# Performance work log

Measured on AMD Instinct MI355X. Metric: run time of the kernel, lower is better.

Reference implementation:

```python
import jax, jax.numpy as jnp
import numpy as np

K = 6  # kernel size for all locally connected layers

def lc2d(x, w, b, stride):
    # x: [B,C,H,W]; w: [O,C,oh,ow,K*K]; b: [O,oh,ow]
    oh, ow = w.shape[2], w.shape[3]
    s = stride
    # unfold: stack the K*K shifted strided views -> [B,C,oh,ow,K*K]
    patches = jnp.stack([x[:, :, i:i + (oh - 1) * s + 1:s, j:j + (ow - 1) * s + 1:s]
                         for i in range(K) for j in range(K)], axis=-1)
    out = jnp.einsum('bchwk,ochwk->bohw', patches, w)
    return out + b[None]

def maxpool2(x):
    # MaxPool2d(2), floor mode: crop odd trailing row/col then 2x2 max
    B, C, H, W = x.shape
    x = x[:, :, : (H // 2) * 2, : (W // 2) * 2]
    return x.reshape(B, C, H // 2, 2, W // 2, 2).max(axis=(3, 5))

def setup_inputs() -> dict:
    key = jax.random.key(0)
    ks = jax.random.split(key, 9)
    f = lambda k, sh: jax.random.normal(k, sh, dtype=jnp.float32) * 0.05
    return {
        'x':  jax.random.normal(ks[0], (16, 3, 218, 178), dtype=jnp.float32),
        'w1': f(ks[1], (8, 3, 213, 173, 36)),  'b1': f(ks[2], (8, 213, 173)),
        'w2': f(ks[3], (16, 8, 51, 41, 36)),   'b2': f(ks[4], (16, 51, 41)),
        'w3': f(ks[5], (32, 16, 16, 12, 36)),  'b3': f(ks[6], (32, 16, 12)),
        'wf': f(ks[7], (10178, 6144)),         'bf': f(ks[8], (10178,)),
    }

def reference(x, w1, b1, w2, b2, w3, b3, wf, bf):
    h = jax.nn.relu(lc2d(x, w1, b1, stride=1))   # [B,8,213,173]
    h = maxpool2(h)                               # [B,8,106,86]
    h = jax.nn.relu(lc2d(h, w2, b2, stride=2))   # [B,16,51,41]
    h = jax.nn.relu(lc2d(h, w3, b3, stride=3))   # [B,32,16,12]
    h = h.reshape(h.shape[0], -1)                 # [B,6144]
    return h @ wf.T + bf                          # [B,10178]
```

## Files before the change

kernel.cpp:

```cpp
#include <hip/hip_runtime.h>

static __device__ __forceinline__ void fma4(float4& a, float s, float4 v) {
  a.x = fmaf(s, v.x, a.x);
  a.y = fmaf(s, v.y, a.y);
  a.z = fmaf(s, v.z, a.z);
  a.w = fmaf(s, v.w, a.w);
}
static __device__ __forceinline__ float4 relu4(float4 a) {
  return make_float4(fmaxf(a.x, 0.f), fmaxf(a.y, 0.f),
                     fmaxf(a.z, 0.f), fmaxf(a.w, 0.f));
}
typedef float floatv4 __attribute__((ext_vector_type(4)));
static __device__ __forceinline__ float4 ntld4(const float* p) {
  floatv4 v = __builtin_nontemporal_load(reinterpret_cast<const floatv4*>(p));
  return make_float4(v.x, v.y, v.z, v.w);
}
typedef float f32x4v __attribute__((ext_vector_type(4)));
typedef short bf16x8 __attribute__((ext_vector_type(8)));
static __device__ __forceinline__ unsigned short f2bf(float f) {
  unsigned u = __float_as_uint(f);
  return (unsigned short)((u + 0x7FFFu + ((u >> 16) & 1u)) >> 16);
}

__global__ void k_transpose(const float* __restrict__ x, float* __restrict__ xt,
                            int chw, int total) {
  int p = blockIdx.x * blockDim.x + threadIdx.x;
  if (p >= total) return;
  float v[16];
#pragma unroll
  for (int b = 0; b < 16; ++b) v[b] = x[(size_t)b * chw + p];
  float4* o4 = reinterpret_cast<float4*>(xt) + (size_t)p * 4;
#pragma unroll
  for (int q = 0; q < 4; ++q)
    o4[q] = make_float4(v[4 * q + 0], v[4 * q + 1], v[4 * q + 2], v[4 * q + 3]);
}

__global__ __launch_bounds__(256, 4) void k_lc1_mfma(
    const float* __restrict__ xt, const float* __restrict__ wgt,
    const float* __restrict__ bias, float* __restrict__ out) {
  constexpr int C = 3, IH = 218, IW = 178, OH = 213, OW = 173;
  constexpr int POS = OH * OW;
  constexpr int KP = 136;
  constexpr int CSTR = IH * IW * 16;
  __shared__ unsigned short wl[16 * 8 * KP];

  const int tid = threadIdx.x;
  const int p0 = blockIdx.x * 16;

  for (int i = tid; i < 3456; i += 256) {
    int pos = i / 216;
    int r = i % 216;
    int o = r / 27;
    int rr = r % 27;
    int c = rr / 9;
    int g4 = rr % 9;
    int gpos = p0 + pos;
    if (gpos >= POS) gpos = POS - 1;
    float4 v = *reinterpret_cast<const float4*>(
        wgt + ((size_t)(o * C + c) * POS + gpos) * 36 + g4 * 4);
    int k0 = (g4 < 8) ? (c * 32 + g4 * 4) : (96 + c * 4);
    unsigned short* d = &wl[(pos * 8 + o) * KP + k0];
    d[0] = f2bf(v.x); d[1] = f2bf(v.y); d[2] = f2bf(v.z); d[3] = f2bf(v.w);
  }
  for (int i = tid; i < 3584; i += 256) {
    int row = i / 28;
    int q = i % 28;
    wl[row * KP + 108 + q] = 0;
  }
  __syncthreads();

  const int l = tid & 63;
  const int wid = tid >> 6;
  const int g = l >> 4;
  const int bb = l & 15;
  const int orow = l & 7;

  int base[8];
  int off3[8];
  bool v3[8];
#pragma unroll
  for (int j = 0; j < 8; ++j) {
    int tap = g * 8 + j;
    base[j] = ((tap / 6) * IW + (tap % 6)) * 16;
    int q = g * 8 + j;
    bool v = (q < 12);
    int cc = v ? (q >> 2) : 0;
    int t3 = v ? (32 + (q & 3)) : 32;
    off3[j] = (cc * IH + 5) * IW * 16 + ((t3 - 30)) * 16;
    v3[j] = v;
  }

  for (int pp = 0; pp < 4; ++pp) {
    int gpos = p0 + wid * 4 + pp;
    bool valid = gpos < POS;
    int cg = valid ? gpos : POS - 1;
    int h = cg / OW, w = cg % OW;
    int posoff = (h * IW + w) * 16 + bb;
    int lpos = wid * 4 + pp;

    f32x4v acc;
#pragma unroll
    for (int j = 0; j < 4; ++j) {
      int o = g * 4 + j;
      acc[j] = (g < 2) ? bias[(size_t)o * POS + cg] : 0.f;
    }

#pragma unroll
    for (int ch = 0; ch < 4; ++ch) {
      bf16x8 a = *reinterpret_cast<const bf16x8*>(
          &wl[(lpos * 8 + orow) * KP + ch * 32 + g * 8]);
      bf16x8 b;
#pragma unroll
      for (int j = 0; j < 8; ++j) {
        float xv;
        if (ch < 3)
          xv = xt[posoff + ch * CSTR + base[j]];
        else
          xv = v3[j] ? xt[posoff + off3[j]] : 0.f;
        b[j] = (short)f2bf(xv);
      }
      acc = __builtin_amdgcn_mfma_f32_16x16x32_bf16(a, b, acc, 0, 0, 0);
    }

    if (valid && g < 2) {
#pragma unroll
      for (int j = 0; j < 4; ++j) {
        int o = g * 4 + j;
        out[((size_t)o * POS + cg) * 16 + bb] = fmaxf(acc[j], 0.f);
      }
    }
  }
}

template <int C, int IH, int IW, int OH, int OW, int S, int O_TOT>
__global__ __launch_bounds__(256) void k_lc_lds_part(
    const float* __restrict__ xt, const float* __restrict__ wgt,
    float* __restrict__ part) {
  constexpr int POS = OH * OW;
  constexpr int NT = (POS + 63) / 64;
  constexpr int OGN = O_TOT / 4;
  __shared__ float4 wl[4 * 64 * 9];
  int tile = blockIdx.x % NT;
  int rem = blockIdx.x / NT;
  int ob0 = (rem % OGN) * 4;
  int c = rem / OGN;
  int p0 = tile * 64;
  int PN = (POS - p0) < 64 ? (POS - p0) : 64;
  int lp = threadIdx.x >> 2, bq = threadIdx.x & 3;
  int fp = p0 + lp;
  bool act = lp < PN;
  int h = act ? fp / OW : 0;
  int w = act ? fp % OW : 0;

  const float4* x4 = reinterpret_cast<const float4*>(xt);
  const float4* w4 = reinterpret_cast<const float4*>(wgt);

  for (int i = threadIdx.x; i < 2304; i += 256) {
    int o_l = i / 576;
    int r = i % 576;
    int pos = r / 9;
    int k4 = r % 9;
    if (pos < PN)
      wl[(o_l * 64 + pos) * 9 + k4] =
          w4[((size_t)((ob0 + o_l) * C + c) * POS + p0 + pos) * 9 + k4];
  }
  __syncthreads();
  if (!act) return;

  float4 acc[4];
#pragma unroll
  for (int o = 0; o < 4; ++o) acc[o] = make_float4(0.f, 0.f, 0.f, 0.f);

  const float4* xc = x4 + ((size_t)(c * IH + h * S) * IW + w * S) * 4 + bq;
#pragma unroll
  for (int k4 = 0; k4 < 9; ++k4) {
    float4 xv[4];
#pragma unroll
    for (int r = 0; r < 4; ++r) {
      int k = k4 * 4 + r;
      xv[r] = xc[((k / 6) * IW + (k % 6)) * 4];
    }
#pragma unroll
    for (int o = 0; o < 4; ++o) {
      float4 wv = wl[(o * 64 + lp) * 9 + k4];
      fma4(acc[o], wv.x, xv[0]);
      fma4(acc[o], wv.y, xv[1]);
      fma4(acc[o], wv.z, xv[2]);
      fma4(acc[o], wv.w, xv[3]);
    }
  }
  float4* pp = reinterpret_cast<float4*>(part) + (size_t)c * (O_TOT * POS * 4);
#pragma unroll
  for (int o = 0; o < 4; ++o)
    pp[((size_t)(ob0 + o) * POS + fp) * 4 + bq] = acc[o];
}

template <int CC, bool A3T>
__global__ void k_combine(const float* __restrict__ part,
                          const float* __restrict__ bias,
                          float* __restrict__ out, int n4total) {
  int p = blockIdx.x * blockDim.x + threadIdx.x;
  if (p >= n4total) return;
  const float4* p4 = reinterpret_cast<const float4*>(part);
  float4 acc = make_float4(0.f, 0.f, 0.f, 0.f);
#pragma unroll
  for (int c = 0; c < CC; ++c) {
    float4 v = p4[(size_t)c * n4total + p];
    acc.x += v.x; acc.y += v.y; acc.z += v.z; acc.w += v.w;
  }
  float bv = bias[p >> 2];
  acc = relu4(make_float4(acc.x + bv, acc.y + bv, acc.z + bv, acc.w + bv));
  if (A3T) {
    int k = p >> 2;
    int bq = p & 3;
    out[(size_t)(bq * 4 + 0) * 6144 + k] = acc.x;
    out[(size_t)(bq * 4 + 1) * 6144 + k] = acc.y;
    out[(size_t)(bq * 4 + 2) * 6144 + k] = acc.z;
    out[(size_t)(bq * 4 + 3) * 6144 + k] = acc.w;
  } else {
    reinterpret_cast<float4*>(out)[p] = acc;
  }
}

__global__ void k_pool(const float* __restrict__ in, float* __restrict__ out,
                       int IH, int IW, int PH, int PW, int total) {
  int t = blockIdx.x * blockDim.x + threadIdx.x;
  if (t >= total) return;
  int bq = t & 3;
  int p = t >> 2;
  int w = p % PW; p /= PW;
  int h = p % PH; p /= PH;
  int o = p;
  const float4* in4 = reinterpret_cast<const float4*>(in);
  size_t r0 = ((size_t)(o * IH + 2 * h) * IW + 2 * w) * 4 + bq;
  float4 a = in4[r0];
  float4 b = in4[r0 + 4];
  float4 c = in4[r0 + (size_t)IW * 4];
  float4 d = in4[r0 + (size_t)IW * 4 + 4];
  float4 m;
  m.x = fmaxf(fmaxf(a.x, b.x), fmaxf(c.x, d.x));
  m.y = fmaxf(fmaxf(a.y, b.y), fmaxf(c.y, d.y));
  m.z = fmaxf(fmaxf(a.z, b.z), fmaxf(c.z, d.z));
  m.w = fmaxf(fmaxf(a.w, b.w), fmaxf(c.w, d.w));
  reinterpret_cast<float4*>(out)[((size_t)(o * PH + h) * PW + w) * 4 + bq] = m;
}

constexpr int FC_N = 10178;
constexpr int FC_K = 6144;
constexpr int FC_KC = 2;
constexpr int FC_KLEN = FC_K / FC_KC;

__global__ __launch_bounds__(256) void k_fc(const float* __restrict__ a3t,
                                            const float* __restrict__ wf,
                                            float* __restrict__ fcp) {
  int wv = threadIdx.x >> 6;
  int l = threadIdx.x & 63;
  int n0 = (blockIdx.x * 4 + wv) * 4;
  int kc = blockIdx.y;
  int kbase = kc * FC_KLEN;

  float acc[64];
#pragma unroll
  for (int j = 0; j < 64; ++j) acc[j] = 0.f;

  int n[4];
#pragma unroll
  for (int m = 0; m < 4; ++m) {
    int nn = n0 + m;
    n[m] = nn < FC_N ? nn : FC_N - 1;
  }

  float4 wr[4];
  {
    int k = kbase + 4 * l;
#pragma unroll
    for (int m = 0; m < 4; ++m) wr[m] = ntld4(wf + (size_t)n[m] * FC_K + k);
  }

  for (int k0 = 0; k0 < FC_KLEN; k0 += 256) {
    int k = kbase + k0 + 4 * l;
    int kp = (k0 + 256 < FC_KLEN) ? (k + 256) : (kbase + 4 * l);
    float4 wrn[4];
#pragma unroll
    for (int m = 0; m < 4; ++m) wrn[m] = ntld4(wf + (size_t)n[m] * FC_K + kp);

#pragma unroll
    for (int bg = 0; bg < 4; ++bg) {
      float4 xv[4];
#pragma unroll
      for (int r = 0; r < 4; ++r)
        xv[r] = *reinterpret_cast<const float4*>(a3t +
                    (size_t)(bg * 4 + r) * FC_K + k);
#pragma unroll
      for (int r = 0; r < 4; ++r) {
        int b = bg * 4 + r;
#pragma unroll
        for (int m = 0; m < 4; ++m) {
          int j = b * 4 + m;
          acc[j] = fmaf(wr[m].x, xv[r].x, acc[j]);
          acc[j] = fmaf(wr[m].y, xv[r].y, acc[j]);
          acc[j] = fmaf(wr[m].z, xv[r].z, acc[j]);
          acc[j] = fmaf(wr[m].w, xv[r].w, acc[j]);
        }
      }
      __builtin_amdgcn_sched_barrier(0);
    }
#pragma unroll
    for (int m = 0; m < 4; ++m) wr[m] = wrn[m];
  }

#pragma unroll
  for (int s = 0; s < 6; ++s) {
    int mask = 1 << s;
    int bit = (l >> s) & 1;
#pragma unroll
    for (int t = 0; t < 32; ++t) {
      if (t < (64 >> (s + 1))) {
        float e = acc[2 * t] + __shfl_xor(acc[2 * t], mask, 64);
        float o = acc[2 * t + 1] + __shfl_xor(acc[2 * t + 1], mask, 64);
        acc[t] = bit ? o : e;
      }
    }
  }

  int b = l >> 2;
  int m = l & 3;
  int nn = n0 + m;
  if (nn < FC_N)
    fcp[((size_t)kc * 16 + b) * FC_N + nn] = acc[0];
}

__global__ void k_fc_comb(const float* __restrict__ fcp,
                          const float* __restrict__ bf,
                          float* __restrict__ out, int total) {
  int t = blockIdx.x * blockDim.x + threadIdx.x;
  if (t >= total) return;
  unsigned n = (unsigned)t % (unsigned)FC_N;
  float s = bf[n];
#pragma unroll
  for (int kc = 0; kc < FC_KC; ++kc) s += fcp[(size_t)kc * 16 * FC_N + t];
  out[t] = s;
}

static inline int cdiv(int a, int b) { return (a + b - 1) / b; }

extern "C" void kernel_launch(void* const* d_in, const int* in_sizes, int n_in,
                              void* d_out, int out_size, void* d_ws,
                              size_t ws_size, hipStream_t stream) {
  const float* x  = (const float*)d_in[0];
  const float* w1 = (const float*)d_in[1];
  const float* b1 = (const float*)d_in[2];
  const float* w2 = (const float*)d_in[3];
  const float* b2 = (const float*)d_in[4];
  const float* w3 = (const float*)d_in[5];
  const float* b3 = (const float*)d_in[6];
  const float* wf = (const float*)d_in[7];
  const float* bf = (const float*)d_in[8];
  float* out = (float*)d_out;

  float* ws = (float*)d_ws;
  float* xt     = ws;
  float* a1     = ws + 1862592;
  float* a1p    = ws + 6579264;
  float* a2     = ws + 7746112;
  float* a3t    = ws + 8281408;
  float* l2part = a1;
  float* l3part = xt;
  float* fcp    = a1p;

  {
    int total = 3 * 218 * 178;
    k_transpose<<<cdiv(total, 256), 256, 0, stream>>>(x, xt, total, total);
  }
  {
    k_lc1_mfma<<<cdiv(213 * 173, 16), 256, 0, stream>>>(xt, w1, b1, a1);
  }
  {
    int total = 4 * 8 * 106 * 86;
    k_pool<<<cdiv(total, 256), 256, 0, stream>>>(a1, a1p, 213, 173, 106, 86,
                                                 total);
  }
  {
    k_lc_lds_part<8, 106, 86, 51, 41, 2, 16>
        <<<33 * 4 * 8, 256, 0, stream>>>(a1p, w2, l2part);
  }
  {
    int n4 = 16 * 2091 * 4;
    k_combine<8, false><<<cdiv(n4, 256), 256, 0, stream>>>(l2part, b2, a2, n4);
  }
  {
    k_lc_lds_part<16, 51, 41, 16, 12, 3, 32>
        <<<3 * 8 * 16, 256, 0, stream>>>(a2, w3, l3part);
  }
  {
    int n4 = 32 * 192 * 4;
    k_combine<16, true><<<cdiv(n4, 256), 256, 0, stream>>>(l3part, b3, a3t, n4);
  }
  {
    dim3 grid(cdiv(FC_N, 16), FC_KC);
    k_fc<<<grid, 256, 0, stream>>>(a3t, wf, fcp);
  }
  {
    int total = 16 * FC_N;
    k_fc_comb<<<cdiv(total, 256), 256, 0, stream>>>(fcp, bf, out, total);
  }
}
```

Baseline: 181.5 us.

## Stage layer-1 input window in LDS as bf16 with row-aligned position tiles

Layer-1 blocks now map to 16 consecutive output columns within a single output row. This lets each block stage the 3x6x21x16 input window, converted to bf16, in shared memory. The MFMA B-operand gathers then read from LDS instead of issuing many scattered global loads and per-element conversions. This adds about 12 KB of LDS per block, drops the occupancy hint from launch bounds, and launches slightly more blocks, some of which are partially idle at the row end.

```diff
diff --git a/kernel.cpp b/kernel.cpp
--- a/kernel.cpp
+++ b/kernel.cpp
@@ -35,17 +35,21 @@
     o4[q] = make_float4(v[4 * q + 0], v[4 * q + 1], v[4 * q + 2], v[4 * q + 3]);
 }
 
-__global__ __launch_bounds__(256, 4) void k_lc1_mfma(
+__global__ __launch_bounds__(256) void k_lc1_mfma(
     const float* __restrict__ xt, const float* __restrict__ wgt,
     const float* __restrict__ bias, float* __restrict__ out) {
   constexpr int C = 3, IH = 218, IW = 178, OH = 213, OW = 173;
   constexpr int POS = OH * OW;
   constexpr int KP = 136;
-  constexpr int CSTR = IH * IW * 16;
+  constexpr int WT = 11;
   __shared__ unsigned short wl[16 * 8 * KP];
+  __shared__ unsigned short xl[18 * 21 * 16];
 
   const int tid = threadIdx.x;
-  const int p0 = blockIdx.x * 16;
+  const int h = blockIdx.x / WT;
+  const int w0 = (blockIdx.x % WT) * 16;
+  const int PN = (OW - w0) < 16 ? (OW - w0) : 16;
+  const int p0 = h * OW + w0;
 
   for (int i = tid; i < 3456; i += 256) {
     int pos = i / 216;
@@ -54,10 +58,9 @@
     int rr = r % 27;
     int c = rr / 9;
     int g4 = rr % 9;
-    int gpos = p0 + pos;
-    if (gpos >= POS) gpos = POS - 1;
+    int pc = pos < PN ? pos : PN - 1;
     float4 v = *reinterpret_cast<const float4*>(
-        wgt + ((size_t)(o * C + c) * POS + gpos) * 36 + g4 * 4);
+        wgt + ((size_t)(o * C + c) * POS + p0 + pc) * 36 + g4 * 4);
     int k0 = (g4 < 8) ? (c * 32 + g4 * 4) : (96 + c * 4);
     unsigned short* d = &wl[(pos * 8 + o) * KP + k0];
     d[0] = f2bf(v.x); d[1] = f2bf(v.y); d[2] = f2bf(v.z); d[3] = f2bf(v.w);
@@ -66,6 +69,16 @@
     int row = i / 28;
     int q = i % 28;
     wl[row * KP + 108 + q] = 0;
+  }
+  for (int i = tid; i < 6048; i += 256) {
+    int seg = i / 336;
+    int rem = i % 336;
+    int wj = rem / 16;
+    int b = rem % 16;
+    int c = seg / 6, ki = seg % 6;
+    int ww = w0 + wj;
+    if (ww > IW - 1) ww = IW - 1;
+    xl[i] = f2bf(xt[((size_t)(c * IH + h + ki) * IW + ww) * 16 + b]);
   }
   __syncthreads();
 
@@ -75,28 +88,27 @@
   const int bb = l & 15;
   const int orow = l & 7;
 
-  int base[8];
-  int off3[8];
+  int koff[8], koff3[8];
   bool v3[8];
 #pragma unroll
   for (int j = 0; j < 8; ++j) {
     int tap = g * 8 + j;
-    base[j] = ((tap / 6) * IW + (tap % 6)) * 16;
+    koff[j] = ((tap / 6) * 21 + (tap % 6)) * 16;
     int q = g * 8 + j;
     bool v = (q < 12);
     int cc = v ? (q >> 2) : 0;
-    int t3 = v ? (32 + (q & 3)) : 32;
-    off3[j] = (cc * IH + 5) * IW * 16 + ((t3 - 30)) * 16;
+    int kj3 = v ? (2 + (q & 3)) : 2;
+    koff3[j] = cc * 2016 + (5 * 21 + kj3) * 16;
     v3[j] = v;
   }
 
+#pragma unroll
   for (int pp = 0; pp < 4; ++pp) {
-    int gpos = p0 + wid * 4 + pp;
-    bool valid = gpos < POS;
-    int cg = valid ? gpos : POS - 1;
-    int h = cg / OW, w = cg % OW;
-    int posoff = (h * IW + w) * 16 + bb;
-    int lpos = wid * 4 + pp;
+    int pos = wid * 4 + pp;
+    bool valid = pos < PN;
+    int cp = valid ? pos : PN - 1;
+    int cg = p0 + cp;
+    int xb = cp * 16 + bb;
 
     f32x4v acc;
 #pragma unroll
@@ -108,18 +120,24 @@
 #pragma unroll
     for (int ch = 0; ch < 4; ++ch) {
       bf16x8 a = *reinterpret_cast<const bf16x8*>(
-          &wl[(lpos * 8 + orow) * KP + ch * 32 + g * 8]);
-      bf16x8 b;
-#pragma unroll
-      for (int j = 0; j < 8; ++j) {
-        float xv;
-        if (ch < 3)
-          xv = xt[posoff + ch * CSTR + base[j]];
-        else
-          xv = v3[j] ? xt[posoff + off3[j]] : 0.f;
-        b[j] = (short)f2bf(xv);
+          &wl[(cp * 8 + orow) * KP + ch * 32 + g * 8]);
+      unsigned short t[8];
+      if (ch < 3) {
+#pragma unroll
+        for (int j = 0; j < 8; ++j) t[j] = xl[ch * 2016 + koff[j] + xb];
+      } else {
+#pragma unroll
+        for (int j = 0; j < 8; ++j)
+          t[j] = v3[j] ? xl[koff3[j] + xb] : (unsigned short)0;
       }
-      acc = __builtin_amdgcn_mfma_f32_16x16x32_bf16(a, b, acc, 0, 0, 0);
+      union {
+        unsigned u[4];
+        bf16x8 v;
+      } B;
+#pragma unroll
+      for (int q = 0; q < 4; ++q)
+        B.u[q] = (unsigned)t[2 * q] | ((unsigned)t[2 * q + 1] << 16);
+      acc = __builtin_amdgcn_mfma_f32_16x16x32_bf16(a, B.v, acc, 0, 0, 0);
     }
 
     if (valid && g < 2) {
@@ -373,7 +391,7 @@
     k_transpose<<<cdiv(total, 256), 256, 0, stream>>>(x, xt, total, total);
   }
   {
-    k_lc1_mfma<<<cdiv(213 * 173, 16), 256, 0, stream>>>(xt, w1, b1, a1);
+    k_lc1_mfma<<<213 * 11, 256, 0, stream>>>(xt, w1, b1, a1);
   }
   {
     int total = 4 * 8 * 106 * 86;
```

Result: slower. 195.7 us (+7.8%).
